# Kernel tuning notes

Hardware: AMD Instinct MI355X
Metric: run time of the kernel (lower is better)

## Reference

```python
import jax, jax.numpy as jnp
import numpy as np

N = 50000
E_RAND = 800000
E = E_RAND + N  # random edges + self loops
IN_DIM = 128
H = 4
D = 32  # num_hidden
HD = H * D  # 128
N_CLS = 2
NEG_SLOPE = 0.2
BN_EPS = 1e-5


def setup_inputs() -> dict:
    key = jax.random.key(0)
    ks = jax.random.split(key, 32)
    x = jax.random.randint(ks[0], (N,), 0, 200)
    src_r = jax.random.randint(ks[1], (E_RAND,), 0, N)
    dst_r = jax.random.randint(ks[2], (E_RAND,), 0, N)
    loops = jnp.arange(N)
    src = jnp.concatenate([src_r, loops])
    dst = jnp.concatenate([dst_r, loops])
    snorm_n = jax.random.uniform(ks[3], (N, 1), jnp.float32, 0.1, 1.0)
    snorm_e = jax.random.uniform(ks[4], (E, 1), jnp.float32, 0.1, 1.0)

    def nrm(k, shape, fan_in):
        return jax.random.normal(k, shape, jnp.float32) * (1.0 / np.sqrt(fan_in))

    inp = {
        'x': x, 'src': src, 'dst': dst, 'snorm_n': snorm_n, 'snorm_e': snorm_e,
        'embed': nrm(ks[5], (200, IN_DIM), 1.0),
        'W0': nrm(ks[6], (IN_DIM, HD), IN_DIM),
        'al0': nrm(ks[7], (H, D), D), 'ar0': nrm(ks[8], (H, D), D),
        'gamma0': jnp.ones((HD,), jnp.float32), 'beta0': jnp.zeros((HD,), jnp.float32),
        'W1': nrm(ks[9], (HD, HD), HD),
        'al1': nrm(ks[10], (H, D), D), 'ar1': nrm(ks[11], (H, D), D),
        'gamma1': jnp.ones((HD,), jnp.float32), 'beta1': jnp.zeros((HD,), jnp.float32),
        'W2': nrm(ks[12], (HD, HD), HD),
        'al2': nrm(ks[13], (H, D), D), 'ar2': nrm(ks[14], (H, D), D),
        'gamma2': jnp.ones((HD,), jnp.float32), 'beta2': jnp.zeros((HD,), jnp.float32),
        'cls1_w': nrm(ks[15], (HD, HD // 2), HD), 'cls1_b': jnp.zeros((HD // 2,), jnp.float32),
        'cls2_w': nrm(ks[16], (HD // 2, N_CLS), HD // 2), 'cls2_b': jnp.zeros((N_CLS,), jnp.float32),
    }
    return inp


def _gat_conv(h, W, al, ar, src, dst, residual, apply_act):
    # h: [N, F_in]; DGL-style GATConv with edge softmax over destination.
    feat = (h @ W).reshape(N, H, D)                         # [N,H,D]
    el = jnp.sum(feat * al, axis=-1)                        # [N,H]
    er = jnp.sum(feat * ar, axis=-1)                        # [N,H]
    e = jax.nn.leaky_relu(el[src] + er[dst], NEG_SLOPE)     # [E,H]
    m = jax.ops.segment_max(e, dst, num_segments=N)         # per-dst max
    ee = jnp.exp(e - m[dst])
    s = jax.ops.segment_sum(ee, dst, num_segments=N)
    a = ee / s[dst]                                         # edge softmax [E,H]
    msg = feat[src] * a[:, :, None]                         # [E,H,D]
    rst = jax.ops.segment_sum(msg, dst, num_segments=N)     # [N,H,D]
    if residual:
        rst = rst + h.reshape(N, H, D)  # identity residual (dims match)
    if apply_act:
        rst = jax.nn.elu(rst)           # activation inside GATConv (layers > 0)
    return rst.reshape(N, HD)


def _bn(h, gamma, beta):
    mu = jnp.mean(h, axis=0)
    var = jnp.mean((h - mu) ** 2, axis=0)  # biased var, matches torch BN training
    return gamma * (h - mu) * jax.lax.rsqrt(var + BN_EPS) + beta


def reference(x, src, dst, snorm_n, snorm_e, embed,
              W0, al0, ar0, gamma0, beta0,
              W1, al1, ar1, gamma1, beta1,
              W2, al2, ar2, gamma2, beta2,
              cls1_w, cls1_b, cls2_w, cls2_b):
    h = embed[x]  # [N, IN_DIM]
    layers = [
        (W0, al0, ar0, gamma0, beta0, False, False),
        (W1, al1, ar1, gamma1, beta1, True, True),
        (W2, al2, ar2, gamma2, beta2, True, True),
    ]
    for W, al, ar, g, b, res, act in layers:
        h = _gat_conv(h, W, al, ar, src, dst, res, act)
        h = h * snorm_n
        h = _bn(h, g, b)
        h = jax.nn.elu(h)
    h = jax.nn.relu(h @ cls1_w + cls1_b)
    logits = h @ cls2_w + cls2_b  # [N, N_CLS]
    return logits
```

## Files before the change

### kernel.cpp

```cpp
#include <hip/hip_runtime.h>
#include <hip/hip_bf16.h>
#include <hip/hip_fp16.h>
#include <math.h>

constexpr int N_NODES = 50000;
constexpr int N_EDGES = 850000;
constexpr int HDIM = 128;
constexpr int AGG_BLOCKS = N_NODES / 8;
constexpr int BN_BUCKETS = 16;

typedef _Float16 f16x8 __attribute__((ext_vector_type(8)));
typedef float f32x4 __attribute__((ext_vector_type(4)));

#define FMAMIX_LO(acc, pk, w) \
    asm("v_fma_mix_f32 %0, %1, %2, %0 op_sel:[0,0,0] op_sel_hi:[1,0,0]" \
        : "+v"(acc) : "v"(pk), "v"(w))
#define FMAMIX_HI(acc, pk, w) \
    asm("v_fma_mix_f32 %0, %1, %2, %0 op_sel:[1,0,0] op_sel_hi:[1,0,0]" \
        : "+v"(acc) : "v"(pk), "v"(w))

__device__ __forceinline__ float elu1(float t) {
    return (t > 0.f) ? t : (__expf(t) - 1.f);
}

constexpr int NB2 = 128;
constexpr int RANGE2 = (N_NODES + NB2 - 1) / NB2;
constexpr int CAP = 8192;
constexpr int CHUNK = 8192;
constexpr int GA = (N_EDGES + CHUNK - 1) / CHUNK;
constexpr int WPACK_BLOCKS = 6;
constexpr int GEMM0_BLOCKS = (N_NODES + 255) / 256;
constexpr int FUSEB_BLOCKS = GEMM0_BLOCKS + NB2;

__global__ void k_fuseA(const int* __restrict__ src, const int* __restrict__ dst,
                        int* __restrict__ g_cursor, unsigned* __restrict__ bucket,
                        const float* __restrict__ W0, const float* __restrict__ W1,
                        const float* __restrict__ W2, __half* __restrict__ wpk,
                        float* __restrict__ bn_part) {
    __shared__ int hist[NB2];
    int tid = threadIdx.x;
    if (blockIdx.x < GA) {
        int e0 = blockIdx.x * CHUNK;
        int e1 = min(e0 + CHUNK, N_EDGES);
        if (tid < NB2) hist[tid] = 0;
        __syncthreads();
        for (int i = e0 + tid; i < e1; i += 1024) {
            int d = dst[i];
            atomicAdd(&hist[d / RANGE2], 1);
        }
        __syncthreads();
        int base = 0;
        if (tid < NB2) base = atomicAdd(&g_cursor[tid], hist[tid]);
        __syncthreads();
        if (tid < NB2) hist[tid] = base;
        __syncthreads();
        for (int i = e0 + tid; i < e1; i += 1024) {
            int d = dst[i];
            int s = src[i];
            int b = d / RANGE2;
            int p = atomicAdd(&hist[b], 1);
            bucket[b * CAP + p] = (unsigned)s | ((unsigned)(d - b * RANGE2) << 16);
        }
    } else {
        int gid = (blockIdx.x - GA) * 1024 + tid;
        int z0 = gid * 8;
        if (z0 < 3 * BN_BUCKETS * 256) {
            float4 z = make_float4(0.f, 0.f, 0.f, 0.f);
            *reinterpret_cast<float4*>(&bn_part[z0]) = z;
            *reinterpret_cast<float4*>(&bn_part[z0 + 4]) = z;
        }
        if (gid >= 3 * 2048) return;
        int L = gid >> 11;
        int rem = gid & 2047;
        int ct = rem >> 8;
        int kc = (rem >> 6) & 3;
        int l = rem & 63;
        const float* W = (L == 0) ? W0 : ((L == 1) ? W1 : W2);
        int c = ct * 16 + (l & 15);
        int k0 = kc * 32 + (l >> 4) * 8;
        __half tmp[8];
#pragma unroll
        for (int j = 0; j < 8; j++) tmp[j] = __float2half(W[(k0 + j) * HDIM + c]);
        *reinterpret_cast<float4*>(&wpk[((size_t)L << 14) +
                                        ((size_t)(ct * 4 + kc) * 64 + l) * 8]) =
            *reinterpret_cast<float4*>(tmp);
    }
}

__global__ void k_fuseB(const int* __restrict__ xidx, const float* __restrict__ embed,
                        const f16x8* __restrict__ wB, __half* __restrict__ feat_h,
                        const float* __restrict__ al, const float* __restrict__ ar,
                        float* __restrict__ el, float* __restrict__ er,
                        const unsigned* __restrict__ bucket, const int* __restrict__ cnts,
                        int* __restrict__ rowstart, int* __restrict__ esrc) {
    __shared__ __align__(16) char smem[16 * 16 * 136 * 2];
    int tid = threadIdx.x;
    if (blockIdx.x < GEMM0_BLOCKS) {
        __half (*sf)[16][136] = reinterpret_cast<__half (*)[16][136]>(smem);
        int w = tid >> 6, lane = tid & 63;
        int r = lane & 15, kg = lane >> 4;
        int wbase = blockIdx.x * 256 + w * 16;
        int n = wbase + r;
        bool ok = n < N_NODES;
        f16x8 aF[4];
#pragma unroll
        for (int kc = 0; kc < 4; kc++)
#pragma unroll
            for (int j = 0; j < 8; j++) aF[kc][j] = (_Float16)0.f;
        if (ok) {
            int xi = xidx[n];
            const float* ep = embed + (size_t)xi * HDIM;
#pragma unroll
            for (int kc = 0; kc < 4; kc++) {
                int c0 = kc * 32 + kg * 8;
                float4 e0 = *reinterpret_cast<const float4*>(ep + c0);
                float4 e1 = *reinterpret_cast<const float4*>(ep + c0 + 4);
                aF[kc][0] = (_Float16)e0.x; aF[kc][1] = (_Float16)e0.y;
                aF[kc][2] = (_Float16)e0.z; aF[kc][3] = (_Float16)e0.w;
                aF[kc][4] = (_Float16)e1.x; aF[kc][5] = (_Float16)e1.y;
                aF[kc][6] = (_Float16)e1.z; aF[kc][7] = (_Float16)e1.w;
            }
        }
        f32x4 acc[8] = {};
#pragma unroll
        for (int kc = 0; kc < 4; kc++) {
#pragma unroll
            for (int ct = 0; ct < 8; ct++) {
                f16x8 bF = wB[(ct * 4 + kc) * 64 + lane];
                acc[ct] = __builtin_amdgcn_mfma_f32_16x16x32_f16(aF[kc], bF, acc[ct], 0, 0, 0);
            }
        }
#pragma unroll
        for (int ct = 0; ct < 8; ct++)
#pragma unroll
            for (int reg = 0; reg < 4; reg++)
                sf[w][kg * 4 + reg][ct * 16 + r] = __float2half(acc[ct][reg]);
        __syncthreads();
        float alq[8], arq[8];
        {
            float4 a0 = *reinterpret_cast<const float4*>(&al[r * 8]);
            float4 a1 = *reinterpret_cast<const float4*>(&al[r * 8 + 4]);
            float4 b0 = *reinterpret_cast<const float4*>(&ar[r * 8]);
            float4 b1 = *reinterpret_cast<const float4*>(&ar[r * 8 + 4]);
            alq[0] = a0.x; alq[1] = a0.y; alq[2] = a0.z; alq[3] = a0.w;
            alq[4] = a1.x; alq[5] = a1.y; alq[6] = a1.z; alq[7] = a1.w;
            arq[0] = b0.x; arq[1] = b0.y; arq[2] = b0.z; arq[3] = b0.w;
            arq[4] = b1.x; arq[5] = b1.y; arq[6] = b1.z; arq[7] = b1.w;
        }
#pragma unroll
        for (int q = 0; q < 4; q++) {
            int row = q * 4 + kg;
            int n2 = wbase + row;
            float4 v = *reinterpret_cast<const float4*>(&sf[w][row][r * 8]);
            if (n2 < N_NODES)
                *reinterpret_cast<float4*>(&feat_h[(size_t)n2 * HDIM + r * 8]) = v;
            const __half2* u = reinterpret_cast<const __half2*>(&v);
            float pl = 0.f, pr = 0.f;
#pragma unroll
            for (int t = 0; t < 4; t++) {
                float lo = __half2float(__low2half(u[t]));
                float hi = __half2float(__high2half(u[t]));
                pl += lo * alq[2 * t] + hi * alq[2 * t + 1];
                pr += lo * arq[2 * t] + hi * arq[2 * t + 1];
            }
            pl += __shfl_xor(pl, 1, 64); pr += __shfl_xor(pr, 1, 64);
            pl += __shfl_xor(pl, 2, 64); pr += __shfl_xor(pr, 2, 64);
            if ((r & 3) == 0 && n2 < N_NODES) {
                int head = r >> 2;
                el[n2 * 4 + head] = pl;
                er[n2 * 4 + head] = pr;
            }
        }
    } else {
        int* cnt_s = reinterpret_cast<int*>(smem);
        int* hist = cnt_s + NB2;
        int* lcur = hist + RANGE2;
        int* wsum = lcur + RANGE2;
        int b = blockIdx.x - GEMM0_BLOCKS;
        int lo = b * RANGE2;
        int myCount = cnts[b];
        if (tid < NB2) cnt_s[tid] = cnts[tid];
        __syncthreads();
        for (int off = 1; off < NB2; off <<= 1) {
            int t = (tid < NB2 && tid >= off) ? cnt_s[tid - off] : 0;
            __syncthreads();
            if (tid < NB2) cnt_s[tid] += t;
            __syncthreads();
        }
        int base = cnt_s[b] - myCount;
        for (int j = tid; j < RANGE2; j += 1024) hist[j] = 0;
        __syncthreads();
        const unsigned* my = bucket + (size_t)b * CAP;
        for (int i = tid; i < myCount; i += 1024) atomicAdd(&hist[my[i] >> 16], 1);
        __syncthreads();
        int v = 0;
        if (tid < 448) v = (tid < RANGE2) ? hist[tid] : 0;
        int inc = v;
        int lane = tid & 63;
#pragma unroll
        for (int off = 1; off < 64; off <<= 1) {
            int t = __shfl_up(inc, off, 64);
            if (lane >= off) inc += t;
        }
        if (tid < 448 && lane == 63) wsum[tid >> 6] = inc;
        __syncthreads();
        if (tid < RANGE2) {
            int woff = 0;
            for (int w = 0; w < (tid >> 6); w++) woff += wsum[w];
            int excl = woff + inc - v;
            lcur[tid] = excl;
            int node = lo + tid;
            if (node < N_NODES) rowstart[node] = base + excl;
        }
        if (b == 0 && tid == 0) rowstart[N_NODES] = N_EDGES;
        __syncthreads();
        for (int i = tid; i < myCount; i += 1024) {
            unsigned p = my[i];
            int pos = atomicAdd(&lcur[p >> 16], 1);
            esrc[base + pos] = (int)(p & 0xFFFFu);
        }
    }
}

__global__ void k_gemm6(const __half* __restrict__ h, const f16x8* __restrict__ wB,
                        __half* __restrict__ feat_h, const float* __restrict__ bn_prev,
                        const float* __restrict__ gamma, const float* __restrict__ beta,
                        const float* __restrict__ al, const float* __restrict__ ar,
                        float* __restrict__ el, float* __restrict__ er) {
    __shared__ __half sf[4][16][136];
    __shared__ __align__(16) float s_sc[128];
    __shared__ __align__(16) float s_sh[128];
    int tid = threadIdx.x;
    {
        float* red = reinterpret_cast<float*>(sf);
        int c = tid & 127, which = tid >> 7;
        float t = 0.f;
#pragma unroll
        for (int b = 0; b < BN_BUCKETS; b++) t += bn_prev[b * 256 + which * 128 + c];
        red[tid] = t;
        __syncthreads();
        if (tid < 128) {
            float mu = red[tid] * (1.f / N_NODES);
            float var = red[128 + tid] * (1.f / N_NODES) - mu * mu;
            float sc = gamma[tid] * rsqrtf(var + 1e-5f);
            s_sc[tid] = sc;
            s_sh[tid] = beta[tid] - mu * sc;
        }
        __syncthreads();
    }
    int w = tid >> 6, lane = tid & 63;
    int r = lane & 15, kg = lane >> 4;
    int wbase = blockIdx.x * 64 + w * 16;
    int n = wbase + r;
    bool ok = n < N_NODES;

    f16x8 aF[4];
#pragma unroll
    for (int kc = 0; kc < 4; kc++)
#pragma unroll
        for (int j = 0; j < 8; j++) aF[kc][j] = (_Float16)0.f;
    if (ok) {
        const __half* hp = h + (size_t)n * HDIM;
#pragma unroll
        for (int kc = 0; kc < 4; kc++) {
            int c0 = kc * 32 + kg * 8;
            float4 raw = *reinterpret_cast<const float4*>(hp + c0);
            const __half2* u = reinterpret_cast<const __half2*>(&raw);
            float4 sc0 = *reinterpret_cast<const float4*>(&s_sc[c0]);
            float4 sc1 = *reinterpret_cast<const float4*>(&s_sc[c0 + 4]);
            float4 sh0 = *reinterpret_cast<const float4*>(&s_sh[c0]);
            float4 sh1 = *reinterpret_cast<const float4*>(&s_sh[c0 + 4]);
            float scv[8] = {sc0.x, sc0.y, sc0.z, sc0.w, sc1.x, sc1.y, sc1.z, sc1.w};
            float shv[8] = {sh0.x, sh0.y, sh0.z, sh0.w, sh1.x, sh1.y, sh1.z, sh1.w};
            float vv[8];
#pragma unroll
            for (int t = 0; t < 4; t++) {
                vv[2 * t] = __half2float(__low2half(u[t]));
                vv[2 * t + 1] = __half2float(__high2half(u[t]));
            }
#pragma unroll
            for (int j = 0; j < 8; j++) {
                float t = vv[j] * scv[j] + shv[j];
                aF[kc][j] = (_Float16)elu1(t);
            }
        }
    }
    __syncthreads();

    f32x4 acc[8] = {};
#pragma unroll
    for (int kc = 0; kc < 4; kc++) {
#pragma unroll
        for (int ct = 0; ct < 8; ct++) {
            f16x8 bF = wB[(ct * 4 + kc) * 64 + lane];
            acc[ct] = __builtin_amdgcn_mfma_f32_16x16x32_f16(aF[kc], bF, acc[ct], 0, 0, 0);
        }
    }

#pragma unroll
    for (int ct = 0; ct < 8; ct++)
#pragma unroll
        for (int reg = 0; reg < 4; reg++)
            sf[w][kg * 4 + reg][ct * 16 + r] = __float2half(acc[ct][reg]);
    __syncthreads();
    float alq[8], arq[8];
    {
        float4 a0 = *reinterpret_cast<const float4*>(&al[r * 8]);
        float4 a1 = *reinterpret_cast<const float4*>(&al[r * 8 + 4]);
        float4 b0 = *reinterpret_cast<const float4*>(&ar[r * 8]);
        float4 b1 = *reinterpret_cast<const float4*>(&ar[r * 8 + 4]);
        alq[0] = a0.x; alq[1] = a0.y; alq[2] = a0.z; alq[3] = a0.w;
        alq[4] = a1.x; alq[5] = a1.y; alq[6] = a1.z; alq[7] = a1.w;
        arq[0] = b0.x; arq[1] = b0.y; arq[2] = b0.z; arq[3] = b0.w;
        arq[4] = b1.x; arq[5] = b1.y; arq[6] = b1.z; arq[7] = b1.w;
    }
#pragma unroll
    for (int q = 0; q < 4; q++) {
        int row = q * 4 + kg;
        int n2 = wbase + row;
        float4 v = *reinterpret_cast<const float4*>(&sf[w][row][r * 8]);
        if (n2 < N_NODES)
            *reinterpret_cast<float4*>(&feat_h[(size_t)n2 * HDIM + r * 8]) = v;
        const __half2* u = reinterpret_cast<const __half2*>(&v);
        float pl = 0.f, pr = 0.f;
#pragma unroll
        for (int t = 0; t < 4; t++) {
            float lo = __half2float(__low2half(u[t]));
            float hi = __half2float(__high2half(u[t]));
            pl += lo * alq[2 * t] + hi * alq[2 * t + 1];
            pr += lo * arq[2 * t] + hi * arq[2 * t + 1];
        }
        pl += __shfl_xor(pl, 1, 64); pr += __shfl_xor(pr, 1, 64);
        pl += __shfl_xor(pl, 2, 64); pr += __shfl_xor(pr, 2, 64);
        if ((r & 3) == 0 && n2 < N_NODES) {
            int head = r >> 2;
            el[n2 * 4 + head] = pl;
            er[n2 * 4 + head] = pr;
        }
    }
}

__global__ void k_agg13(const __half* __restrict__ feat_h, const float* __restrict__ el,
                        const float* __restrict__ er, const int* __restrict__ rowstart,
                        const int* __restrict__ esrc, const float* __restrict__ snorm_n,
                        __half* __restrict__ h, const float* __restrict__ bn_prev,
                        const float* __restrict__ gamma, const float* __restrict__ beta,
                        float* __restrict__ bn_cur, int layer) {
    __shared__ __align__(16) int2 lds[4][2][2][32][4];
    __shared__ __align__(16) float s_sc[128];
    __shared__ __align__(16) float s_sh[128];
    int tid = threadIdx.x;
    if (layer > 0) {
        float* red = reinterpret_cast<float*>(lds);
        int c = tid & 127, which = tid >> 7;
        float t = 0.f;
#pragma unroll
        for (int b = 0; b < BN_BUCKETS; b++) t += bn_prev[b * 256 + which * 128 + c];
        red[tid] = t;
        __syncthreads();
        if (tid < 128) {
            float mu = red[tid] * (1.f / N_NODES);
            float var = red[128 + tid] * (1.f / N_NODES) - mu * mu;
            float sc = gamma[tid] * rsqrtf(var + 1e-5f);
            s_sc[tid] = sc;
            s_sh[tid] = beta[tid] - mu * sc;
        }
        __syncthreads();
    }
    int wave = tid >> 6, lane = tid & 63;
    int h2 = lane >> 5, hl = lane & 31;
    int dp = hl & 15, epair = hl >> 4, head = dp >> 2;
    unsigned dpo = (unsigned)dp << 4;
    const char* fb = reinterpret_cast<const char*>(feat_h);
    const char* eb = reinterpret_cast<const char*>(el);
    int n = blockIdx.x * 8 + wave * 2 + h2;
    int e0 = rowstart[n];
    int deg = rowstart[n + 1] - e0;
    int dmax = max(deg, __shfl_xor(deg, 32, 64));
    float4 er4 = *(const float4*)&er[n * 4];
    float s = 0.f;
    float a[8] = {};
    int nch = (dmax + 31) >> 5;

    int idx0 = e0 + min(hl, deg - 1);
    int sidx_p = esrc[idx0];
    float4 el_p = *reinterpret_cast<const float4*>(eb + ((unsigned)sidx_p << 4));
    bool val_p = hl < deg;

    for (int c = 0; c < nch; c++) {
        float w0 = 0.f, w1 = 0.f, w2 = 0.f, w3 = 0.f;
        int sv = sidx_p;
        if (val_p) {
            float ex = el_p.x + er4.x, ey = el_p.y + er4.y;
            float ez = el_p.z + er4.z, ew = el_p.w + er4.w;
            ex = fmaxf(ex, 0.f) + 0.2f * fminf(ex, 0.f);
            ey = fmaxf(ey, 0.f) + 0.2f * fminf(ey, 0.f);
            ez = fmaxf(ez, 0.f) + 0.2f * fminf(ez, 0.f);
            ew = fmaxf(ew, 0.f) + 0.2f * fminf(ew, 0.f);
            w0 = __expf(ex); w1 = __expf(ey); w2 = __expf(ez); w3 = __expf(ew);
        }
        int4* wp = reinterpret_cast<int4*>(&lds[wave][h2][c & 1][hl][0]);
        wp[0] = make_int4(sv, __float_as_int(w0), sv, __float_as_int(w1));
        wp[1] = make_int4(sv, __float_as_int(w2), sv, __float_as_int(w3));
        if (c + 1 < nch) {
            int slot = (c + 1) * 32 + hl;
            int idx = e0 + min(slot, deg - 1);
            sidx_p = esrc[idx];
            el_p = *reinterpret_cast<const float4*>(eb + ((unsigned)sidx_p << 4));
            val_p = slot < deg;
        }
        int cnt = min(32, dmax - c * 32);
        int iters = (cnt + 1) >> 1;
        int itr8 = (iters + 7) & ~7;
        const int2 (*slot_p)[4] = lds[wave][h2][c & 1];
#pragma unroll 1
        for (int j = 0; j < itr8; j += 8) {
            int2 rr[8];
#pragma unroll
            for (int q = 0; q < 8; q++) rr[q] = slot_p[(j + q) * 2 + epair][head];
            uint4 uu[8];
#pragma unroll
            for (int q = 0; q < 8; q++)
                uu[q] = *reinterpret_cast<const uint4*>(fb + (((unsigned)rr[q].x << 8) + dpo));
#pragma unroll
            for (int q = 0; q < 8; q++) {
                float w = __int_as_float(rr[q].y);
                FMAMIX_LO(a[0], uu[q].x, w); FMAMIX_HI(a[1], uu[q].x, w);
                FMAMIX_LO(a[2], uu[q].y, w); FMAMIX_HI(a[3], uu[q].y, w);
                FMAMIX_LO(a[4], uu[q].z, w); FMAMIX_HI(a[5], uu[q].z, w);
                FMAMIX_LO(a[6], uu[q].w, w); FMAMIX_HI(a[7], uu[q].w, w);
                s += w;
            }
        }
    }
#pragma unroll
    for (int k = 0; k < 8; k++) a[k] += __shfl_xor(a[k], 16, 64);
    s += __shfl_xor(s, 16, 64);
    float r[8] = {};
    if (epair == 0) {
        float inv = 1.f / s;
        int d0 = dp * 8;
#pragma unroll
        for (int k = 0; k < 8; k++) r[k] = a[k] * inv;
        if (layer > 0) {
            float4 hraw = *reinterpret_cast<const float4*>(&h[(size_t)n * HDIM + d0]);
            __half2 q0 = *(__half2*)&hraw.x, q1 = *(__half2*)&hraw.y;
            __half2 q2 = *(__half2*)&hraw.z, q3 = *(__half2*)&hraw.w;
            float hv[8] = {__half2float(__low2half(q0)), __half2float(__high2half(q0)),
                           __half2float(__low2half(q1)), __half2float(__high2half(q1)),
                           __half2float(__low2half(q2)), __half2float(__high2half(q2)),
                           __half2float(__low2half(q3)), __half2float(__high2half(q3))};
            float4 sc0 = *reinterpret_cast<const float4*>(&s_sc[d0]);
            float4 sc1 = *reinterpret_cast<const float4*>(&s_sc[d0 + 4]);
            float4 sh0 = *reinterpret_cast<const float4*>(&s_sh[d0]);
            float4 sh1 = *reinterpret_cast<const float4*>(&s_sh[d0 + 4]);
            float scv[8] = {sc0.x, sc0.y, sc0.z, sc0.w, sc1.x, sc1.y, sc1.z, sc1.w};
            float shv[8] = {sh0.x, sh0.y, sh0.z, sh0.w, sh1.x, sh1.y, sh1.z, sh1.w};
#pragma unroll
            for (int k = 0; k < 8; k++) {
                float t = hv[k] * scv[k] + shv[k];
                r[k] += elu1(t);
                r[k] = elu1(r[k]);
            }
        }
        float sn = snorm_n[n];
#pragma unroll
        for (int k = 0; k < 8; k++) r[k] *= sn;
        float4 outv;
        *(__half2*)&outv.x = __floats2half2_rn(r[0], r[1]);
        *(__half2*)&outv.y = __floats2half2_rn(r[2], r[3]);
        *(__half2*)&outv.z = __floats2half2_rn(r[4], r[5]);
        *(__half2*)&outv.w = __floats2half2_rn(r[6], r[7]);
        *reinterpret_cast<float4*>(&h[(size_t)n * HDIM + d0]) = outv;
    }

    float* bsum = reinterpret_cast<float*>(lds);
    __syncthreads();
    if (epair == 0) {
        int n8 = wave * 2 + h2;
        int cbase = n8 * 128 + dp * 8;
#pragma unroll
        for (int k = 0; k < 8; k++) {
            bsum[cbase + k] = r[k];
            bsum[1024 + cbase + k] = r[k] * r[k];
        }
    }
    __syncthreads();
    {
        int c = tid & 127, which = tid >> 7;
        float v = 0.f;
#pragma unroll
        for (int n8 = 0; n8 < 8; n8++) v += bsum[which * 1024 + n8 * 128 + c];
        atomicAdd(&bn_cur[(blockIdx.x & (BN_BUCKETS - 1)) * 256 + which * 128 + c], v);
    }
}

__global__ void k_classifier(const __half* __restrict__ h, const float* __restrict__ W1,
                             const float* __restrict__ b1, const float* __restrict__ W2,
                             const float* __restrict__ b2, const float* __restrict__ bn_prev,
                             const float* __restrict__ gamma, const float* __restrict__ beta,
                             float* __restrict__ out) {
    __shared__ float hs[16][128];
    __shared__ __align__(16) float s_sc[128];
    __shared__ __align__(16) float s_sh[128];
    int tid = threadIdx.x;
    {
        float* red = &hs[0][0];
        int c = tid & 127, which = tid >> 7;
        float t = 0.f;
#pragma unroll
        for (int b = 0; b < BN_BUCKETS; b++) t += bn_prev[b * 256 + which * 128 + c];
        red[tid] = t;
        __syncthreads();
        if (tid < 128) {
            float mu = red[tid] * (1.f / N_NODES);
            float var = red[128 + tid] * (1.f / N_NODES) - mu * mu;
            float sc = gamma[tid] * rsqrtf(var + 1e-5f);
            s_sc[tid] = sc;
            s_sh[tid] = beta[tid] - mu * sc;
        }
        __syncthreads();
    }
    int nbase = blockIdx.x * 16;
    for (int i = tid; i < 16 * 128; i += 256) {
        int r = i >> 7, c = i & 127;
        int n = nbase + r;
        float v = 0.f;
        if (n < N_NODES) {
            v = __half2float(h[(size_t)n * HDIM + c]) * s_sc[c] + s_sh[c];
            v = elu1(v);
        }
        hs[r][c] = v;
    }
    __syncthreads();
    int j = tid & 63;
    int g = tid >> 6;
    float bj = b1[j];
    float acc[4] = {bj, bj, bj, bj};
    for (int k = 0; k < 128; k++) {
        float w = W1[k * 64 + j];
#pragma unroll
        for (int i = 0; i < 4; i++) acc[i] += hs[g * 4 + i][k] * w;
    }
    float w20 = W2[j * 2], w21 = W2[j * 2 + 1];
    float res[8];
#pragma unroll
    for (int i = 0; i < 4; i++) {
        float hid = fmaxf(acc[i], 0.f);
        res[2 * i] = hid * w20;
        res[2 * i + 1] = hid * w21;
    }
#pragma unroll
    for (int off = 1; off < 64; off <<= 1)
#pragma unroll
        for (int i = 0; i < 8; i++) res[i] += __shfl_xor(res[i], off, 64);
    if (j < 8) {
        int n = nbase + g * 4 + (j >> 1);
        if (n < N_NODES) out[n * 2 + (j & 1)] = res[j] + b2[j & 1];
    }
}

extern "C" void kernel_launch(void* const* d_in, const int* in_sizes, int n_in,
                              void* d_out, int out_size, void* d_ws, size_t ws_size,
                              hipStream_t stream) {
    const int* x = (const int*)d_in[0];
    const int* src = (const int*)d_in[1];
    const int* dst = (const int*)d_in[2];
    const float* snorm_n = (const float*)d_in[3];
    const float* embed = (const float*)d_in[5];
    const float* Ws[3] = {(const float*)d_in[6], (const float*)d_in[11], (const float*)d_in[16]};
    const float* als[3] = {(const float*)d_in[7], (const float*)d_in[12], (const float*)d_in[17]};
    const float* ars[3] = {(const float*)d_in[8], (const float*)d_in[13], (const float*)d_in[18]};
    const float* gms[3] = {(const float*)d_in[9], (const float*)d_in[14], (const float*)d_in[19]};
    const float* bts[3] = {(const float*)d_in[10], (const float*)d_in[15], (const float*)d_in[20]};
    const float* cls1_w = (const float*)d_in[21];
    const float* cls1_b = (const float*)d_in[22];
    const float* cls2_w = (const float*)d_in[23];
    const float* cls2_b = (const float*)d_in[24];
    float* out = (float*)d_out;

    char* ws = (char*)d_ws;
    size_t off = 0;
    auto alloc = [&](size_t bytes) {
        void* p = ws + off;
        off = (off + bytes + 255) & ~(size_t)255;
        return p;
    };
    __half* h = (__half*)alloc((size_t)N_NODES * HDIM * 2);
    __half* feat_h = (__half*)alloc((size_t)N_NODES * HDIM * 2);
    float* el = (float*)alloc((size_t)N_NODES * 4 * 4);
    float* er = (float*)alloc((size_t)N_NODES * 4 * 4);
    int* rowstart = (int*)alloc((size_t)(N_NODES + 1) * 4);
    int* esrc = (int*)alloc((size_t)N_EDGES * 4);
    int* g_cursor = (int*)alloc((size_t)NB2 * 4);
    float* bn_part = (float*)alloc((size_t)3 * BN_BUCKETS * 256 * 4);
    __half* wpkh = (__half*)alloc((size_t)3 * 16384 * 2);
    unsigned* g_bucket = (unsigned*)alloc((size_t)NB2 * CAP * 4);
    (void)ws_size; (void)in_sizes; (void)n_in; (void)out_size;

    hipMemsetAsync(g_cursor, 0, NB2 * 4, stream);
    k_fuseA<<<GA + WPACK_BLOCKS, 1024, 0, stream>>>(src, dst, g_cursor, g_bucket,
                                                    Ws[0], Ws[1], Ws[2], wpkh, bn_part);
    k_fuseB<<<FUSEB_BLOCKS, 1024, 0, stream>>>(x, embed,
                                               reinterpret_cast<const f16x8*>(wpkh),
                                               feat_h, als[0], ars[0], el, er,
                                               g_bucket, g_cursor, rowstart, esrc);
    k_agg13<<<AGG_BLOCKS, 256, 0, stream>>>(feat_h, el, er, rowstart, esrc,
                                            snorm_n, h, bn_part, gms[0], bts[0],
                                            bn_part, 0);
    for (int L = 1; L < 3; L++) {
        const f16x8* wB = reinterpret_cast<const f16x8*>(wpkh + ((size_t)L << 14));
        const float* bn_prev = bn_part + (size_t)(L - 1) * BN_BUCKETS * 256;
        float* bn_cur = bn_part + (size_t)L * BN_BUCKETS * 256;
        k_gemm6<<<(N_NODES + 63) / 64, 256, 0, stream>>>(h, wB, feat_h,
                                                         bn_prev, gms[L - 1], bts[L - 1],
                                                         als[L], ars[L], el, er);
        k_agg13<<<AGG_BLOCKS, 256, 0, stream>>>(feat_h, el, er, rowstart, esrc,
                                                snorm_n, h, bn_prev, gms[L - 1], bts[L - 1],
                                                bn_cur, L);
    }

    k_classifier<<<(N_NODES + 15) / 16, 256, 0, stream>>>(h, cls1_w, cls1_b, cls2_w, cls2_b,
                                                          bn_part + (size_t)2 * BN_BUCKETS * 256,
                                                          gms[2], bts[2], out);
}
```

Before: 311.8 us.

## Move classifier hidden layer to MFMA with prepacked fp16 weights; shrink agg unroll

The classifier's first linear layer now runs as 16x16x32 fp16 MFMA tiles over 64 nodes per block. The fp16 cls1 weights are packed once in the setup kernel, in the same layout as the GAT weights. This replaces the scalar shared-memory FMA loop, which reread fp32 weights for every 16 nodes. The second layer is reduced with 16-lane shuffles. Separately, the aggregation inner loop gathers 4 edges per batch instead of 8, which cuts padding waste and register pressure at the cost of less memory-level parallelism. The classifier's hidden layer now uses fp16 inputs and weights, which costs some precision.

After: 293.4 us. -5.9%, faster.

```diff
diff --git a/kernel.cpp b/kernel.cpp
--- a/kernel.cpp
+++ b/kernel.cpp
@@ -28,14 +28,15 @@
 constexpr int CAP = 8192;
 constexpr int CHUNK = 8192;
 constexpr int GA = (N_EDGES + CHUNK - 1) / CHUNK;
-constexpr int WPACK_BLOCKS = 6;
+constexpr int WPACK_BLOCKS = 7;
 constexpr int GEMM0_BLOCKS = (N_NODES + 255) / 256;
 constexpr int FUSEB_BLOCKS = GEMM0_BLOCKS + NB2;
 
 __global__ void k_fuseA(const int* __restrict__ src, const int* __restrict__ dst,
                         int* __restrict__ g_cursor, unsigned* __restrict__ bucket,
                         const float* __restrict__ W0, const float* __restrict__ W1,
-                        const float* __restrict__ W2, __half* __restrict__ wpk,
+                        const float* __restrict__ W2, const float* __restrict__ cls1w,
+                        __half* __restrict__ wpk, __half* __restrict__ wcls,
                         float* __restrict__ bn_part) {
     __shared__ int hist[NB2];
     int tid = threadIdx.x;
@@ -69,21 +70,34 @@
             *reinterpret_cast<float4*>(&bn_part[z0]) = z;
             *reinterpret_cast<float4*>(&bn_part[z0 + 4]) = z;
         }
-        if (gid >= 3 * 2048) return;
-        int L = gid >> 11;
-        int rem = gid & 2047;
-        int ct = rem >> 8;
-        int kc = (rem >> 6) & 3;
-        int l = rem & 63;
-        const float* W = (L == 0) ? W0 : ((L == 1) ? W1 : W2);
-        int c = ct * 16 + (l & 15);
-        int k0 = kc * 32 + (l >> 4) * 8;
-        __half tmp[8];
-#pragma unroll
-        for (int j = 0; j < 8; j++) tmp[j] = __float2half(W[(k0 + j) * HDIM + c]);
-        *reinterpret_cast<float4*>(&wpk[((size_t)L << 14) +
-                                        ((size_t)(ct * 4 + kc) * 64 + l) * 8]) =
-            *reinterpret_cast<float4*>(tmp);
+        if (gid < 3 * 2048) {
+            int L = gid >> 11;
+            int rem = gid & 2047;
+            int ct = rem >> 8;
+            int kc = (rem >> 6) & 3;
+            int l = rem & 63;
+            const float* W = (L == 0) ? W0 : ((L == 1) ? W1 : W2);
+            int c = ct * 16 + (l & 15);
+            int k0 = kc * 32 + (l >> 4) * 8;
+            __half tmp[8];
+#pragma unroll
+            for (int j = 0; j < 8; j++) tmp[j] = __float2half(W[(k0 + j) * HDIM + c]);
+            *reinterpret_cast<float4*>(&wpk[((size_t)L << 14) +
+                                            ((size_t)(ct * 4 + kc) * 64 + l) * 8]) =
+                *reinterpret_cast<float4*>(tmp);
+        } else if (gid < 3 * 2048 + 1024) {
+            int g2 = gid - 3 * 2048;
+            int ct = g2 >> 8;
+            int kc = (g2 >> 6) & 3;
+            int l = g2 & 63;
+            int c = ct * 16 + (l & 15);
+            int k0 = kc * 32 + (l >> 4) * 8;
+            __half tmp[8];
+#pragma unroll
+            for (int j = 0; j < 8; j++) tmp[j] = __float2half(cls1w[(k0 + j) * 64 + c]);
+            *reinterpret_cast<float4*>(&wcls[((size_t)(ct * 4 + kc) * 64 + l) * 8]) =
+                *reinterpret_cast<float4*>(tmp);
+        }
     }
 }
 
@@ -340,7 +354,7 @@
     }
 }
 
-__global__ void k_agg13(const __half* __restrict__ feat_h, const float* __restrict__ el,
+__global__ void k_agg14(const __half* __restrict__ feat_h, const float* __restrict__ el,
                         const float* __restrict__ er, const int* __restrict__ rowstart,
                         const int* __restrict__ esrc, const float* __restrict__ snorm_n,
                         __half* __restrict__ h, const float* __restrict__ bn_prev,
@@ -411,19 +425,19 @@
         }
         int cnt = min(32, dmax - c * 32);
         int iters = (cnt + 1) >> 1;
-        int itr8 = (iters + 7) & ~7;
+        int itr4 = (iters + 3) & ~3;
         const int2 (*slot_p)[4] = lds[wave][h2][c & 1];
 #pragma unroll 1
-        for (int j = 0; j < itr8; j += 8) {
-            int2 rr[8];
-#pragma unroll
-            for (int q = 0; q < 8; q++) rr[q] = slot_p[(j + q) * 2 + epair][head];
-            uint4 uu[8];
-#pragma unroll
-            for (int q = 0; q < 8; q++)
+        for (int j = 0; j < itr4; j += 4) {
+            int2 rr[4];
+#pragma unroll
+            for (int q = 0; q < 4; q++) rr[q] = slot_p[(j + q) * 2 + epair][head];
+            uint4 uu[4];
+#pragma unroll
+            for (int q = 0; q < 4; q++)
                 uu[q] = *reinterpret_cast<const uint4*>(fb + (((unsigned)rr[q].x << 8) + dpo));
 #pragma unroll
-            for (int q = 0; q < 8; q++) {
+            for (int q = 0; q < 4; q++) {
                 float w = __int_as_float(rr[q].y);
                 FMAMIX_LO(a[0], uu[q].x, w); FMAMIX_HI(a[1], uu[q].x, w);
                 FMAMIX_LO(a[2], uu[q].y, w); FMAMIX_HI(a[3], uu[q].y, w);
@@ -495,17 +509,16 @@
     }
 }
 
-__global__ void k_classifier(const __half* __restrict__ h, const float* __restrict__ W1,
-                             const float* __restrict__ b1, const float* __restrict__ W2,
-                             const float* __restrict__ b2, const float* __restrict__ bn_prev,
-                             const float* __restrict__ gamma, const float* __restrict__ beta,
-                             float* __restrict__ out) {
-    __shared__ float hs[16][128];
+__global__ void k_classifier2(const __half* __restrict__ h, const f16x8* __restrict__ w1B,
+                              const float* __restrict__ b1, const float* __restrict__ W2,
+                              const float* __restrict__ b2, const float* __restrict__ bn_prev,
+                              const float* __restrict__ gamma, const float* __restrict__ beta,
+                              float* __restrict__ out) {
+    __shared__ float red[256];
     __shared__ __align__(16) float s_sc[128];
     __shared__ __align__(16) float s_sh[128];
     int tid = threadIdx.x;
     {
-        float* red = &hs[0][0];
         int c = tid & 127, which = tid >> 7;
         float t = 0.f;
 #pragma unroll
@@ -521,42 +534,85 @@
         }
         __syncthreads();
     }
-    int nbase = blockIdx.x * 16;
-    for (int i = tid; i < 16 * 128; i += 256) {
-        int r = i >> 7, c = i & 127;
-        int n = nbase + r;
-        float v = 0.f;
-        if (n < N_NODES) {
-            v = __half2float(h[(size_t)n * HDIM + c]) * s_sc[c] + s_sh[c];
-            v = elu1(v);
-        }
-        hs[r][c] = v;
-    }
-    __syncthreads();
-    int j = tid & 63;
-    int g = tid >> 6;
-    float bj = b1[j];
-    float acc[4] = {bj, bj, bj, bj};
-    for (int k = 0; k < 128; k++) {
-        float w = W1[k * 64 + j];
-#pragma unroll
-        for (int i = 0; i < 4; i++) acc[i] += hs[g * 4 + i][k] * w;
-    }
-    float w20 = W2[j * 2], w21 = W2[j * 2 + 1];
-    float res[8];
-#pragma unroll
-    for (int i = 0; i < 4; i++) {
-        float hid = fmaxf(acc[i], 0.f);
-        res[2 * i] = hid * w20;
-        res[2 * i + 1] = hid * w21;
-    }
-#pragma unroll
-    for (int off = 1; off < 64; off <<= 1)
-#pragma unroll
-        for (int i = 0; i < 8; i++) res[i] += __shfl_xor(res[i], off, 64);
-    if (j < 8) {
-        int n = nbase + g * 4 + (j >> 1);
-        if (n < N_NODES) out[n * 2 + (j & 1)] = res[j] + b2[j & 1];
+    int w = tid >> 6, lane = tid & 63;
+    int r = lane & 15, kg = lane >> 4;
+    int wbase = blockIdx.x * 64 + w * 16;
+    int n = wbase + r;
+    bool ok = n < N_NODES;
+
+    f16x8 aF[4];
+#pragma unroll
+    for (int kc = 0; kc < 4; kc++)
+#pragma unroll
+        for (int j = 0; j < 8; j++) aF[kc][j] = (_Float16)0.f;
+    if (ok) {
+        const __half* hp = h + (size_t)n * HDIM;
+#pragma unroll
+        for (int kc = 0; kc < 4; kc++) {
+            int c0 = kc * 32 + kg * 8;
+            float4 raw = *reinterpret_cast<const float4*>(hp + c0);
+            const __half2* u = reinterpret_cast<const __half2*>(&raw);
+            float4 sc0 = *reinterpret_cast<const float4*>(&s_sc[c0]);
+            float4 sc1 = *reinterpret_cast<const float4*>(&s_sc[c0 + 4]);
+            float4 sh0 = *reinterpret_cast<const float4*>(&s_sh[c0]);
+            float4 sh1 = *reinterpret_cast<const float4*>(&s_sh[c0 + 4]);
+            float scv[8] = {sc0.x, sc0.y, sc0.z, sc0.w, sc1.x, sc1.y, sc1.z, sc1.w};
+            float shv[8] = {sh0.x, sh0.y, sh0.z, sh0.w, sh1.x, sh1.y, sh1.z, sh1.w};
+            float vv[8];
+#pragma unroll
+            for (int t = 0; t < 4; t++) {
+                vv[2 * t] = __half2float(__low2half(u[t]));
+                vv[2 * t + 1] = __half2float(__high2half(u[t]));
+            }
+#pragma unroll
+            for (int j = 0; j < 8; j++) {
+                float t = vv[j] * scv[j] + shv[j];
+                aF[kc][j] = (_Float16)elu1(t);
+            }
+        }
+    }
+
+    f32x4 acc[4] = {};
+#pragma unroll
+    for (int kc = 0; kc < 4; kc++) {
+#pragma unroll
+        for (int ct = 0; ct < 4; ct++) {
+            f16x8 bF = w1B[(ct * 4 + kc) * 64 + lane];
+            acc[ct] = __builtin_amdgcn_mfma_f32_16x16x32_f16(aF[kc], bF, acc[ct], 0, 0, 0);
+        }
+    }
+
+    float b1q[4], w20q[4], w21q[4];
+#pragma unroll
+    for (int ct = 0; ct < 4; ct++) {
+        int c = ct * 16 + r;
+        b1q[ct] = b1[c];
+        float2 w2v = *reinterpret_cast<const float2*>(&W2[c * 2]);
+        w20q[ct] = w2v.x;
+        w21q[ct] = w2v.y;
+    }
+    float b20 = b2[0], b21 = b2[1];
+#pragma unroll
+    for (int reg = 0; reg < 4; reg++) {
+        float p0 = 0.f, p1 = 0.f;
+#pragma unroll
+        for (int ct = 0; ct < 4; ct++) {
+            float hid = fmaxf(acc[ct][reg] + b1q[ct], 0.f);
+            p0 += hid * w20q[ct];
+            p1 += hid * w21q[ct];
+        }
+#pragma unroll
+        for (int off = 1; off < 16; off <<= 1) {
+            p0 += __shfl_xor(p0, off, 64);
+            p1 += __shfl_xor(p1, off, 64);
+        }
+        if (r == 0) {
+            int n2 = wbase + kg * 4 + reg;
+            if (n2 < N_NODES) {
+                out[n2 * 2] = p0 + b20;
+                out[n2 * 2 + 1] = p1 + b21;
+            }
+        }
     }
 }
 
@@ -595,17 +651,19 @@
     int* g_cursor = (int*)alloc((size_t)NB2 * 4);
     float* bn_part = (float*)alloc((size_t)3 * BN_BUCKETS * 256 * 4);
     __half* wpkh = (__half*)alloc((size_t)3 * 16384 * 2);
+    __half* wcls = (__half*)alloc((size_t)8192 * 2);
     unsigned* g_bucket = (unsigned*)alloc((size_t)NB2 * CAP * 4);
     (void)ws_size; (void)in_sizes; (void)n_in; (void)out_size;
 
     hipMemsetAsync(g_cursor, 0, NB2 * 4, stream);
     k_fuseA<<<GA + WPACK_BLOCKS, 1024, 0, stream>>>(src, dst, g_cursor, g_bucket,
-                                                    Ws[0], Ws[1], Ws[2], wpkh, bn_part);
+                                                    Ws[0], Ws[1], Ws[2], cls1_w,
+                                                    wpkh, wcls, bn_part);
     k_fuseB<<<FUSEB_BLOCKS, 1024, 0, stream>>>(x, embed,
                                                reinterpret_cast<const f16x8*>(wpkh),
                                                feat_h, als[0], ars[0], el, er,
                                                g_bucket, g_cursor, rowstart, esrc);
-    k_agg13<<<AGG_BLOCKS, 256, 0, stream>>>(feat_h, el, er, rowstart, esrc,
+    k_agg14<<<AGG_BLOCKS, 256, 0, stream>>>(feat_h, el, er, rowstart, esrc,
                                             snorm_n, h, bn_part, gms[0], bts[0],
                                             bn_part, 0);
     for (int L = 1; L < 3; L++) {
@@ -615,12 +673,14 @@
         k_gemm6<<<(N_NODES + 63) / 64, 256, 0, stream>>>(h, wB, feat_h,
                                                          bn_prev, gms[L - 1], bts[L - 1],
                                                          als[L], ars[L], el, er);
-        k_agg13<<<AGG_BLOCKS, 256, 0, stream>>>(feat_h, el, er, rowstart, esrc,
+        k_agg14<<<AGG_BLOCKS, 256, 0, stream>>>(feat_h, el, er, rowstart, esrc,
                                                 snorm_n, h, bn_prev, gms[L - 1], bts[L - 1],
                                                 bn_cur, L);
     }
 
-    k_classifier<<<(N_NODES + 15) / 16, 256, 0, stream>>>(h, cls1_w, cls1_b, cls2_w, cls2_b,
-                                                          bn_part + (size_t)2 * BN_BUCKETS * 256,
-                                                          gms[2], bts[2], out);
+    k_classifier2<<<(N_NODES + 63) / 64, 256, 0, stream>>>(h,
+                                                           reinterpret_cast<const f16x8*>(wcls),
+                                                           cls1_b, cls2_w, cls2_b,
+                                                           bn_part + (size_t)2 * BN_BUCKETS * 256,
+                                                           gms[2], bts[2], out);
 }
```
